# Kernel optimization log

Hardware: AMD Instinct MI355X
Metric: run time of the kernel (lower is better)

The kernel has to match this reference:

```python
import jax, jax.numpy as jnp
import numpy as np

N, F, HID, H, B = 400000, 128, 32, 4, 2000

def setup_inputs() -> dict:
    key = jax.random.key(0)
    ks = jax.random.split(key, 8)
    atom_fea = jax.random.normal(ks[0], (N, F), dtype=jnp.float32)
    segment_ids = jnp.sort(jax.random.randint(ks[1], (N,), 0, B, dtype=jnp.int32))
    s = 0.05
    return {
        "atom_fea": atom_fea,
        "segment_ids": segment_ids,
        "num_crystals": B,
        "W1": jax.random.normal(ks[2], (F, HID), dtype=jnp.float32) * s,
        "b1": jnp.zeros((HID,), dtype=jnp.float32),
        "W2": jax.random.normal(ks[3], (HID, H), dtype=jnp.float32) * s,
        "b2": jnp.zeros((H,), dtype=jnp.float32),
        "Wp": jax.random.normal(ks[4], (H * F, F), dtype=jnp.float32) * s,
        "bp": jnp.zeros((F,), dtype=jnp.float32),
    }

def reference(atom_fea, segment_ids, num_crystals, W1, b1, W2, b2, Wp, bp):
    # key MLP: (N,F) -> (N,H) attention logits (dropout is eval no-op)
    logits = jax.nn.silu(atom_fea @ W1 + b1) @ W2 + b2  # (N,H)
    # segment softmax over atoms within each crystal, per head
    seg_max = jax.ops.segment_max(logits, segment_ids, num_segments=num_crystals)
    ex = jnp.exp(logits - seg_max[segment_ids])
    denom = jax.ops.segment_sum(ex, segment_ids, num_segments=num_crystals)
    w = ex / denom[segment_ids]  # (N,H)
    # per-head softmax-weighted segment sum of atom features -> (B,H,F)
    weighted = jax.ops.segment_sum(
        w[:, :, None] * atom_fea[:, None, :], segment_ids, num_segments=num_crystals
    )
    flat = weighted.reshape(num_crystals, -1)  # (B, H*F)
    return jax.nn.silu(flat @ Wp + bp)  # (B,F)
```

## Files before the change

kernel.cpp:

```cpp
#include <hip/hip_runtime.h>
#include <math.h>

#define F 128
#define HID 32
#define NH 4
#define TILE 32
#define ROWB 512
#define PJC 4

typedef __attribute__((ext_vector_type(8))) short bf16x8;
typedef __attribute__((ext_vector_type(4))) float f32x4;

__device__ __forceinline__ float silu_f(float x) {
    return x / (1.0f + __expf(-x));
}

__device__ __forceinline__ uint f2bf(float f) {
    union { float f; uint u; } v; v.f = f;
    uint r = v.u + 0x7fffu + ((v.u >> 16) & 1u);
    return r >> 16;
}

__device__ __forceinline__ uint cvtpk_bf16(float lo, float hi) {
    uint r;
    asm("v_cvt_pk_bf16_f32 %0, %1, %2" : "=v"(r) : "v"(lo), "v"(hi));
    return r;
}

__device__ __forceinline__ void gload_lds16(const void* g, void* l) {
    __builtin_amdgcn_global_load_lds(
        (const __attribute__((address_space(1))) void*)g,
        (__attribute__((address_space(3))) void*)l, 16, 0, 0);
}

__global__ void seg_starts_kernel(const int* __restrict__ seg, int* __restrict__ starts,
                                  int N, int B) {
    int i = blockIdx.x * blockDim.x + threadIdx.x;
    if (i >= N) return;
    int id = seg[i];
    if (i == 0) {
        for (int b = 0; b <= id; ++b) starts[b] = 0;
    } else {
        int prev = seg[i - 1];
        for (int b = prev + 1; b <= id; ++b) starts[b] = i;
    }
    if (i == N - 1) {
        for (int b = id + 1; b <= B; ++b) starts[b] = N;
    }
}

__global__ __launch_bounds__(256, 4) void fused9_kernel(
    const float* __restrict__ atom_fea, const int* __restrict__ starts,
    const float* __restrict__ W1, const float* __restrict__ b1,
    const float* __restrict__ W2, const float* __restrict__ b2,
    float* __restrict__ gWacc) {
    __shared__ float sStage[2][TILE * F];
    __shared__ float sP[2 * TILE * 5];
    __shared__ float sTW[NH * 65];

    const int t = threadIdx.x;
    const int b = blockIdx.x;
    const int start = starts[b];
    const int end = starts[b + 1];
    const int wv = t >> 6;
    const int lane = t & 63;
    const int lg = lane >> 4;
    const int l15 = lane & 15;
    const int ag = wv & 1;
    const int mh = wv >> 1;
    const int ca = lane & 3;
    const int co = (lane >> 2) & 15;

    int roff[4], coff[4];
    #pragma unroll
    for (int i = 0; i < 4; ++i) {
        const int q = i * 256 + t;
        roff[i] = q >> 5;
        coff[i] = ((q & 31) ^ (roff[i] & 7)) << 4;
    }

    bf16x8 w1f[4];
    #pragma unroll
    for (int kk = 0; kk < 4; ++kk) {
        bf16x8 fr;
        #pragma unroll
        for (int j = 0; j < 8; ++j)
            fr[j] = (short)f2bf(W1[(kk * 32 + lg * 8 + j) * HID + mh * 16 + l15]);
        w1f[kk] = fr;
    }
    float b1r[4], w2r[4][4];
    #pragma unroll
    for (int r = 0; r < 4; ++r) {
        const int h = mh * 16 + lg * 4 + r;
        b1r[r] = b1[h];
        #pragma unroll
        for (int j = 0; j < 4; ++j) w2r[r][j] = W2[h * NH + j];
    }
    const float b2w = b2[wv];

    float m_run = -INFINITY;
    float s_part = 0.0f;
    float acc8[8] = {0, 0, 0, 0, 0, 0, 0, 0};

    const int nt = (end > start) ? (end - start + TILE - 1) / TILE : 0;
    const char* gbase = (const char*)atom_fea;

    if (nt > 0) {
        #pragma unroll
        for (int i = 0; i < 4; ++i) {
            int a = start + roff[i]; a = (a < end) ? a : end - 1;
            gload_lds16(gbase + (size_t)a * ROWB + coff[i],
                        (char*)sStage[0] + i * 4096 + wv * 1024);
        }
    }
    __syncthreads();

    int pb = 0;
    for (int ti = 0; ti < nt; ++ti) {
        const int base = start + ti * TILE;
        const int T = min(TILE, end - base);
        const char* bufc = (const char*)sStage[pb];
        const bool has_next = (ti + 1 < nt);

        if (has_next) {
            const int nbase = base + TILE;
            char* ldst = (char*)sStage[pb ^ 1];
            #pragma unroll
            for (int i = 0; i < 4; ++i) {
                int a = nbase + roff[i]; a = (a < end) ? a : end - 1;
                gload_lds16(gbase + (size_t)a * ROWB + coff[i],
                            ldst + i * 4096 + wv * 1024);
            }
        }

        {
            f32x4 acc;
            #pragma unroll
            for (int r = 0; r < 4; ++r) acc[r] = b1r[r];
            const int row = ag * 16 + l15;
            const char* rb = bufc + row * ROWB;
            const int rs = row & 7;
            #pragma unroll
            for (int kk = 0; kk < 4; ++kk) {
                const int c0 = kk * 8 + lg * 2;
                const float4 va = *(const float4*)(rb + ((c0 ^ rs) << 4));
                const float4 vb = *(const float4*)(rb + (((c0 + 1) ^ rs) << 4));
                union { bf16x8 v; uint u[4]; } fr;
                fr.u[0] = cvtpk_bf16(va.x, va.y);
                fr.u[1] = cvtpk_bf16(va.z, va.w);
                fr.u[2] = cvtpk_bf16(vb.x, vb.y);
                fr.u[3] = cvtpk_bf16(vb.z, vb.w);
                acc = __builtin_amdgcn_mfma_f32_16x16x32_bf16(w1f[kk], fr.v, acc, 0, 0, 0);
            }
            float p0 = 0, p1 = 0, p2 = 0, p3 = 0;
            #pragma unroll
            for (int r = 0; r < 4; ++r) {
                const float s = silu_f(acc[r]);
                p0 = fmaf(s, w2r[r][0], p0);
                p1 = fmaf(s, w2r[r][1], p1);
                p2 = fmaf(s, w2r[r][2], p2);
                p3 = fmaf(s, w2r[r][3], p3);
            }
            p0 += __shfl_xor(p0, 16); p0 += __shfl_xor(p0, 32);
            p1 += __shfl_xor(p1, 16); p1 += __shfl_xor(p1, 32);
            p2 += __shfl_xor(p2, 16); p2 += __shfl_xor(p2, 32);
            p3 += __shfl_xor(p3, 16); p3 += __shfl_xor(p3, 32);
            if (lane < 16) {
                float* d = &sP[(mh * TILE + ag * 16 + lane) * 5];
                d[0] = p0; d[1] = p1; d[2] = p2; d[3] = p3;
            }
        }
        asm volatile("s_waitcnt lgkmcnt(0)" ::: "memory");
        __builtin_amdgcn_s_barrier();

        {
            const float v = (lane < T)
                ? sP[lane * 5 + wv] + sP[(TILE + lane) * 5 + wv] + b2w
                : -INFINITY;
            if (__any(v > m_run + 8.0f)) {
                float mt = v;
                #pragma unroll
                for (int d = 1; d < 64; d <<= 1) mt = fmaxf(mt, __shfl_xor(mt, d));
                const float m_new = fmaxf(m_run, mt);
                const float r = __expf(m_run - m_new);
                s_part *= r;
                #pragma unroll
                for (int j = 0; j < 8; ++j) acc8[j] *= r;
                m_run = m_new;
            }
            const float e = (lane < T) ? __expf(v - m_run) : 0.0f;
            sTW[wv * 65 + lane] = e;
            s_part += e;
        }

        {
            #pragma unroll 4
            for (int i = 0; i < 8; ++i) {
                const int a = i * 4 + ca;
                const float w = sTW[wv * 65 + a];
                const int sw = a & 7;
                const char* ra = bufc + a * ROWB;
                const float4 v0 = *(const float4*)(ra + (((2 * co) ^ sw) << 4));
                const float4 v1 = *(const float4*)(ra + (((2 * co + 1) ^ sw) << 4));
                acc8[0] = fmaf(w, v0.x, acc8[0]);
                acc8[1] = fmaf(w, v0.y, acc8[1]);
                acc8[2] = fmaf(w, v0.z, acc8[2]);
                acc8[3] = fmaf(w, v0.w, acc8[3]);
                acc8[4] = fmaf(w, v1.x, acc8[4]);
                acc8[5] = fmaf(w, v1.y, acc8[5]);
                acc8[6] = fmaf(w, v1.z, acc8[6]);
                acc8[7] = fmaf(w, v1.w, acc8[7]);
            }
        }
        __syncthreads();
        pb ^= 1;
    }

    #pragma unroll
    for (int d = 1; d < 64; d <<= 1) s_part += __shfl_xor(s_part, d);
    const float inv = (s_part > 0.0f) ? 1.0f / s_part : 0.0f;
    #pragma unroll
    for (int j = 0; j < 8; ++j) {
        acc8[j] += __shfl_xor(acc8[j], 1);
        acc8[j] += __shfl_xor(acc8[j], 2);
    }
    if ((lane & 3) == 0) {
        float* dst = &gWacc[(size_t)b * 512 + wv * F + (lane >> 2) * 8];
        *(float4*)dst = make_float4(acc8[0] * inv, acc8[1] * inv, acc8[2] * inv, acc8[3] * inv);
        *(float4*)(dst + 4) = make_float4(acc8[4] * inv, acc8[5] * inv, acc8[6] * inv, acc8[7] * inv);
    }
}

__global__ __launch_bounds__(256) void proj_kernel(
    const float* __restrict__ gWacc, const float* __restrict__ Wp,
    const float* __restrict__ bp, float* __restrict__ out, int B) {
    __shared__ float sW[PJC * 512];
    __shared__ float sP[256 * PJC];
    const int t = threadIdx.x;
    const int c0 = blockIdx.x * PJC;
    for (int q = t; q < PJC * 512; q += 256) {
        const int cr = c0 + (q >> 9);
        sW[q] = (cr < B) ? gWacc[(size_t)cr * 512 + (q & 511)] : 0.0f;
    }
    __syncthreads();
    const int f = t & 127, half = t >> 7;
    float acc[PJC] = {};
    const float* wp = Wp + (size_t)(half * 256) * F + f;
    for (int k0 = 0; k0 < 256; k0 += 8) {
        float wpv[8];
        #pragma unroll
        for (int u = 0; u < 8; ++u) wpv[u] = wp[(size_t)(k0 + u) * F];
        #pragma unroll
        for (int u = 0; u < 8; ++u) {
            const int ks = half * 256 + k0 + u;
            #pragma unroll
            for (int g = 0; g < PJC; ++g) acc[g] = fmaf(sW[g * 512 + ks], wpv[u], acc[g]);
        }
    }
    #pragma unroll
    for (int g = 0; g < PJC; ++g) sP[t * PJC + g] = acc[g];
    __syncthreads();
    if (t < 128) {
        const float bpf = bp[t];
        #pragma unroll
        for (int g = 0; g < PJC; ++g) {
            const int cr = c0 + g;
            if (cr < B)
                out[(size_t)cr * F + t] =
                    silu_f(sP[t * PJC + g] + sP[(t + 128) * PJC + g] + bpf);
        }
    }
}

extern "C" void kernel_launch(void* const* d_in, const int* in_sizes, int n_in,
                              void* d_out, int out_size, void* d_ws, size_t ws_size,
                              hipStream_t stream) {
    const float* atom_fea = (const float*)d_in[0];
    const int* seg = (const int*)d_in[1];
    const float* W1 = (const float*)d_in[3];
    const float* b1 = (const float*)d_in[4];
    const float* W2 = (const float*)d_in[5];
    const float* b2 = (const float*)d_in[6];
    const float* Wp = (const float*)d_in[7];
    const float* bp = (const float*)d_in[8];
    float* out = (float*)d_out;

    const int N = in_sizes[0] / F;
    const int B = out_size / F;

    char* ws = (char*)d_ws;
    int* starts = (int*)ws;
    size_t off = (((size_t)(B + 1) * sizeof(int)) + 255) & ~(size_t)255;
    float* gWacc = (float*)(ws + off);

    seg_starts_kernel<<<(N + 255) / 256, 256, 0, stream>>>(seg, starts, N, B);
    fused9_kernel<<<B, 256, 0, stream>>>(atom_fea, starts, W1, b1, W2, b2, gWacc);
    proj_kernel<<<(B + PJC - 1) / PJC, 256, 0, stream>>>(gWacc, Wp, bp, out, B);
}
```

Before: 64.72 us.

## Triple-buffer atom tiles with prefetch distance two and counted waits

Expands the LDS staging from two to three tile buffers so global-to-LDS loads run two tiles ahead of compute. The full __syncthreads is replaced by explicit s_waitcnt vmcnt counts plus s_barrier, so a wave waits only for the tile about to be consumed. This targets exposed memory latency in the streaming pass over atom features. The extra LDS per block may reduce how many blocks fit per CU.

```diff
diff --git a/kernel.cpp b/kernel.cpp
--- a/kernel.cpp
+++ b/kernel.cpp
@@ -49,12 +49,12 @@
     }
 }
 
-__global__ __launch_bounds__(256, 4) void fused9_kernel(
+__global__ __launch_bounds__(256, 4) void fused14_kernel(
     const float* __restrict__ atom_fea, const int* __restrict__ starts,
     const float* __restrict__ W1, const float* __restrict__ b1,
     const float* __restrict__ W2, const float* __restrict__ b2,
     float* __restrict__ gWacc) {
-    __shared__ float sStage[2][TILE * F];
+    __shared__ float sStage[3][TILE * F];
     __shared__ float sP[2 * TILE * 5];
     __shared__ float sTW[NH * 65];
 
@@ -113,18 +113,30 @@
                         (char*)sStage[0] + i * 4096 + wv * 1024);
         }
     }
-    __syncthreads();
-
-    int pb = 0;
+    if (nt > 1) {
+        #pragma unroll
+        for (int i = 0; i < 4; ++i) {
+            int a = start + TILE + roff[i]; a = (a < end) ? a : end - 1;
+            gload_lds16(gbase + (size_t)a * ROWB + coff[i],
+                        (char*)sStage[1] + i * 4096 + wv * 1024);
+        }
+        asm volatile("s_waitcnt vmcnt(4)" ::: "memory");
+    } else {
+        asm volatile("s_waitcnt vmcnt(0)" ::: "memory");
+    }
+    __builtin_amdgcn_s_barrier();
+
+    int cur = 0;
     for (int ti = 0; ti < nt; ++ti) {
         const int base = start + ti * TILE;
         const int T = min(TILE, end - base);
-        const char* bufc = (const char*)sStage[pb];
-        const bool has_next = (ti + 1 < nt);
-
-        if (has_next) {
-            const int nbase = base + TILE;
-            char* ldst = (char*)sStage[pb ^ 1];
+        const char* bufc = (const char*)sStage[cur];
+        const int nx2 = (cur == 0) ? 2 : (cur - 1);
+
+        const bool has2 = (ti + 2 < nt);
+        if (has2) {
+            const int nbase = base + 2 * TILE;
+            char* ldst = (char*)sStage[nx2];
             #pragma unroll
             for (int i = 0; i < 4; ++i) {
                 int a = nbase + roff[i]; a = (a < end) ? a : end - 1;
@@ -212,8 +224,16 @@
                 acc8[7] = fmaf(w, v1.w, acc8[7]);
             }
         }
-        __syncthreads();
-        pb ^= 1;
+
+        if (ti + 1 < nt) {
+            if (has2) {
+                asm volatile("s_waitcnt vmcnt(4) lgkmcnt(0)" ::: "memory");
+            } else {
+                asm volatile("s_waitcnt vmcnt(0) lgkmcnt(0)" ::: "memory");
+            }
+            __builtin_amdgcn_s_barrier();
+        }
+        cur = (cur == 2) ? 0 : (cur + 1);
     }
 
     #pragma unroll
@@ -294,6 +314,6 @@
     float* gWacc = (float*)(ws + off);
 
     seg_starts_kernel<<<(N + 255) / 256, 256, 0, stream>>>(seg, starts, N, B);
-    fused9_kernel<<<B, 256, 0, stream>>>(atom_fea, starts, W1, b1, W2, b2, gWacc);
+    fused14_kernel<<<B, 256, 0, stream>>>(atom_fea, starts, W1, b1, W2, b2, gWacc);
     proj_kernel<<<(B + PJC - 1) / PJC, 256, 0, stream>>>(gWacc, Wp, bp, out, B);
 }
```

After: 65.93 us. About the same (+1.9%).

## Process two crystals per block with continuous prefetch across segment boundary

Applied to the files above, without the earlier changes.

Each block of the fused attention-pooling kernel now handles two consecutive crystals and walks their tiles in one loop. The double-buffered prefetch runs straight across the crystal boundary, and the softmax state is finalized and reset when a crystal's last tile completes. This halves the grid size and amortizes per-block setup (W1/W2 fragment loads, first-tile pipeline fill) over two segments. The cost is fewer blocks for load balancing, plus extra index arithmetic and a warp reduction inside the loop body.

```diff
diff --git a/kernel.cpp b/kernel.cpp
--- a/kernel.cpp
+++ b/kernel.cpp
@@ -7,6 +7,7 @@
 #define TILE 32
 #define ROWB 512
 #define PJC 4
+#define CPB 2
 
 typedef __attribute__((ext_vector_type(8))) short bf16x8;
 typedef __attribute__((ext_vector_type(4))) float f32x4;
@@ -49,19 +50,18 @@
     }
 }
 
-__global__ __launch_bounds__(256, 4) void fused9_kernel(
+__global__ __launch_bounds__(256, 4) void fused15_kernel(
     const float* __restrict__ atom_fea, const int* __restrict__ starts,
     const float* __restrict__ W1, const float* __restrict__ b1,
     const float* __restrict__ W2, const float* __restrict__ b2,
-    float* __restrict__ gWacc) {
+    float* __restrict__ gWacc, int B) {
     __shared__ float sStage[2][TILE * F];
     __shared__ float sP[2 * TILE * 5];
     __shared__ float sTW[NH * 65];
 
     const int t = threadIdx.x;
-    const int b = blockIdx.x;
-    const int start = starts[b];
-    const int end = starts[b + 1];
+    const int bid = blockIdx.x;
+    const int b0 = bid * CPB;
     const int wv = t >> 6;
     const int lane = t & 63;
     const int lg = lane >> 4;
@@ -71,6 +71,16 @@
     const int ca = lane & 3;
     const int co = (lane >> 2) & 15;
 
+    int cst[CPB], cen[CPB], cnt[CPB];
+    #pragma unroll
+    for (int c = 0; c < CPB; ++c) {
+        const int bb = b0 + c;
+        if (bb < B) { cst[c] = starts[bb]; cen[c] = starts[bb + 1]; }
+        else { cst[c] = 0; cen[c] = 0; }
+        cnt[c] = (cen[c] > cst[c]) ? (cen[c] - cst[c] + TILE - 1) / TILE : 0;
+    }
+    const int total = cnt[0] + cnt[1];
+
     int roff[4], coff[4];
     #pragma unroll
     for (int i = 0; i < 4; ++i) {
@@ -102,13 +112,15 @@
     float s_part = 0.0f;
     float acc8[8] = {0, 0, 0, 0, 0, 0, 0, 0};
 
-    const int nt = (end > start) ? (end - start + TILE - 1) / TILE : 0;
     const char* gbase = (const char*)atom_fea;
 
-    if (nt > 0) {
+    if (total > 0) {
+        const int ci = (cnt[0] > 0) ? 0 : 1;
+        const int base0 = cst[ci];
+        const int end0 = cen[ci];
         #pragma unroll
         for (int i = 0; i < 4; ++i) {
-            int a = start + roff[i]; a = (a < end) ? a : end - 1;
+            int a = base0 + roff[i]; a = (a < end0) ? a : end0 - 1;
             gload_lds16(gbase + (size_t)a * ROWB + coff[i],
                         (char*)sStage[0] + i * 4096 + wv * 1024);
         }
@@ -116,18 +128,23 @@
     __syncthreads();
 
     int pb = 0;
-    for (int ti = 0; ti < nt; ++ti) {
-        const int base = start + ti * TILE;
+    for (int j = 0; j < total; ++j) {
+        const int cj = (j < cnt[0]) ? 0 : 1;
+        const int tl = (j < cnt[0]) ? j : j - cnt[0];
+        const int base = cst[cj] + tl * TILE;
+        const int end = cen[cj];
         const int T = min(TILE, end - base);
         const char* bufc = (const char*)sStage[pb];
-        const bool has_next = (ti + 1 < nt);
-
-        if (has_next) {
-            const int nbase = base + TILE;
+
+        if (j + 1 < total) {
+            const int cn = (j + 1 < cnt[0]) ? 0 : 1;
+            const int tn = (j + 1 < cnt[0]) ? (j + 1) : (j + 1 - cnt[0]);
+            const int nbase = cst[cn] + tn * TILE;
+            const int nend = cen[cn];
             char* ldst = (char*)sStage[pb ^ 1];
             #pragma unroll
             for (int i = 0; i < 4; ++i) {
-                int a = nbase + roff[i]; a = (a < end) ? a : end - 1;
+                int a = nbase + roff[i]; a = (a < nend) ? a : nend - 1;
                 gload_lds16(gbase + (size_t)a * ROWB + coff[i],
                             ldst + i * 4096 + wv * 1024);
             }
@@ -185,7 +202,7 @@
                 const float r = __expf(m_run - m_new);
                 s_part *= r;
                 #pragma unroll
-                for (int j = 0; j < 8; ++j) acc8[j] *= r;
+                for (int q = 0; q < 8; ++q) acc8[q] *= r;
                 m_run = m_new;
             }
             const float e = (lane < T) ? __expf(v - m_run) : 0.0f;
@@ -212,22 +229,40 @@
                 acc8[7] = fmaf(w, v1.w, acc8[7]);
             }
         }
+
+        if (tl == cnt[cj] - 1) {
+            #pragma unroll
+            for (int d = 1; d < 64; d <<= 1) s_part += __shfl_xor(s_part, d);
+            const float inv = (s_part > 0.0f) ? 1.0f / s_part : 0.0f;
+            #pragma unroll
+            for (int q = 0; q < 8; ++q) {
+                acc8[q] += __shfl_xor(acc8[q], 1);
+                acc8[q] += __shfl_xor(acc8[q], 2);
+            }
+            if ((lane & 3) == 0) {
+                float* dst = &gWacc[(size_t)(b0 + cj) * 512 + wv * F + (lane >> 2) * 8];
+                *(float4*)dst = make_float4(acc8[0] * inv, acc8[1] * inv,
+                                            acc8[2] * inv, acc8[3] * inv);
+                *(float4*)(dst + 4) = make_float4(acc8[4] * inv, acc8[5] * inv,
+                                                  acc8[6] * inv, acc8[7] * inv);
+            }
+            m_run = -INFINITY;
+            s_part = 0.0f;
+            #pragma unroll
+            for (int q = 0; q < 8; ++q) acc8[q] = 0.0f;
+        }
+
         __syncthreads();
         pb ^= 1;
     }
 
     #pragma unroll
-    for (int d = 1; d < 64; d <<= 1) s_part += __shfl_xor(s_part, d);
-    const float inv = (s_part > 0.0f) ? 1.0f / s_part : 0.0f;
-    #pragma unroll
-    for (int j = 0; j < 8; ++j) {
-        acc8[j] += __shfl_xor(acc8[j], 1);
-        acc8[j] += __shfl_xor(acc8[j], 2);
-    }
-    if ((lane & 3) == 0) {
-        float* dst = &gWacc[(size_t)b * 512 + wv * F + (lane >> 2) * 8];
-        *(float4*)dst = make_float4(acc8[0] * inv, acc8[1] * inv, acc8[2] * inv, acc8[3] * inv);
-        *(float4*)(dst + 4) = make_float4(acc8[4] * inv, acc8[5] * inv, acc8[6] * inv, acc8[7] * inv);
+    for (int c = 0; c < CPB; ++c) {
+        if (cnt[c] == 0 && (b0 + c) < B && (lane & 3) == 0) {
+            float* dst = &gWacc[(size_t)(b0 + c) * 512 + wv * F + (lane >> 2) * 8];
+            *(float4*)dst = make_float4(0.f, 0.f, 0.f, 0.f);
+            *(float4*)(dst + 4) = make_float4(0.f, 0.f, 0.f, 0.f);
+        }
     }
 }
 
@@ -294,6 +329,7 @@
     float* gWacc = (float*)(ws + off);
 
     seg_starts_kernel<<<(N + 255) / 256, 256, 0, stream>>>(seg, starts, N, B);
-    fused9_kernel<<<B, 256, 0, stream>>>(atom_fea, starts, W1, b1, W2, b2, gWacc);
+    fused15_kernel<<<(B + CPB - 1) / CPB, 256, 0, stream>>>(atom_fea, starts, W1, b1,
+                                                            W2, b2, gWacc, B);
     proj_kernel<<<(B + PJC - 1) / PJC, 256, 0, stream>>>(gWacc, Wp, bp, out, B);
 }
```

New measurement: 68.54 us. +5.9%, slower.
